# Optimization experiments

Measured on AMD Instinct MI355X. Metric: run time of the kernel, lower is better.

Reference implementation:

```python
import jax, jax.numpy as jnp
import numpy as np

NUM_PER_PATH = 16
MARGIN_INTRA = 0.1
MARGIN_INTER = 1.0


def setup_inputs() -> dict:
    key = jax.random.key(0)
    # [B, block_num, 1, 1, 2]; trailing dims must multiply to 2 (see _get_center view)
    path_fea = jax.random.normal(key, (131072, 64, 1, 1, 2), dtype=jnp.float32)
    return {"path_fea": path_fea}


def reference(path_fea):
    B, block = path_fea.shape[0], path_fea.shape[1]
    D = block * 2                     # flattened per-sample feature dim
    G = B // NUM_PER_PATH             # number of centers (groups)
    fea = path_fea.reshape(B, D)      # [B, D] (matches path_fea[j].view(-1))

    # center: mean over the NUM_PER_PATH samples of each group, per block
    # (identical math to the permute/view dance in _get_center)
    grouped = fea.reshape(G, NUM_PER_PATH, D)          # [G, P, D]
    center = jnp.mean(grouped, axis=1)                 # [G, D]

    # ---- inter loss: hinge on pairwise euclidean distances between centers ----
    sq = jnp.sum(center * center, axis=1)              # [G]
    gram = center @ center.T                           # [G, G]
    d2 = jnp.maximum(sq[:, None] + sq[None, :] - 2.0 * gram, 0.0)
    pair_mask = jnp.triu(jnp.ones((G, G), dtype=bool), k=1)  # i < j
    d = jnp.sqrt(jnp.where(pair_mask, d2, 1.0))        # safe sqrt off-mask
    hinge = jnp.maximum(MARGIN_INTER - d, 0.0) ** 2
    n_pairs = G * (G - 1) / 2.0
    inter_loss = jnp.sum(jnp.where(pair_mask, hinge, 0.0)) / n_pairs

    # ---- intra loss: hinge on distance of each sample to its group center ----
    diff = grouped - center[:, None, :]                # [G, P, D]
    di = jnp.sqrt(jnp.sum(diff * diff, axis=-1))       # [G, P]
    intra_loss = jnp.sum(jnp.maximum(di - MARGIN_INTRA, 0.0) ** 2) / (G * NUM_PER_PATH)

    return (inter_loss, intra_loss)
```

## Files before the change

kernel.cpp:

```cpp
#include <hip/hip_runtime.h>
#include <hip/hip_bf16.h>
#include <math.h>

#define B_ROWS   131072
#define D_DIM    128
#define P_SAMP   16
#define G_GROUPS 8192
#define T128     64
#define NTRI2    2080
#define K1_BLOCKS (G_GROUPS / 4)

typedef __bf16 bf16x8  __attribute__((ext_vector_type(8)));
typedef float  floatx4 __attribute__((ext_vector_type(4)));
typedef unsigned short u16x8 __attribute__((ext_vector_type(8)));


__device__ __forceinline__ float wave_red64(float v) {
    #pragma unroll
    for (int off = 32; off > 0; off >>= 1) v += __shfl_xor(v, off, 64);
    return v;
}

template <int CTRL>
__device__ __forceinline__ float dpp_ror_add(float v) {
    int r = __builtin_amdgcn_update_dpp(0, __builtin_bit_cast(int, v),
                                        CTRL, 0xf, 0xf, false);
    return v + __builtin_bit_cast(float, r);
}
__device__ __forceinline__ float row16_sum(float v) {
    v = dpp_ror_add<0x121>(v);
    v = dpp_ror_add<0x122>(v);
    v = dpp_ror_add<0x124>(v);
    v = dpp_ror_add<0x128>(v);
    return v;
}

__global__ __launch_bounds__(256) void k_center_intra(
    const float* __restrict__ x,
    uint2* __restrict__ cfrag,
    float* __restrict__ sq,
    float* __restrict__ partial,
    float* __restrict__ acc)
{
    const int wave = threadIdx.x >> 6;
    const int lane = threadIdx.x & 63;
    const int half = lane >> 5;
    const int c    = lane & 31;
    const int g    = blockIdx.x * 4 + wave;

    if (blockIdx.x == 0 && threadIdx.x == 0) acc[0] = 0.f;

    const float* base = x + (size_t)g * (P_SAMP * D_DIM) + half * D_DIM + c * 4;

    floatx4 v[8];
    #pragma unroll
    for (int l = 0; l < 8; ++l)
        v[l] = *(const floatx4*)(base + l * (2 * D_DIM));

    floatx4 cs = v[0];
    #pragma unroll
    for (int l = 1; l < 8; ++l) cs += v[l];
    #pragma unroll
    for (int k = 0; k < 4; ++k) cs[k] += __shfl_xor(cs[k], 32, 64);
    floatx4 ctr = cs * (1.0f / P_SAMP);

    float p[9];
    #pragma unroll
    for (int l = 0; l < 8; ++l) {
        floatx4 d = v[l] - ctr;
        p[l] = d[0]*d[0] + d[1]*d[1] + d[2]*d[2] + d[3]*d[3];
    }
    p[8] = ctr[0]*ctr[0] + ctr[1]*ctr[1] + ctr[2]*ctr[2] + ctr[3]*ctr[3];

    #pragma unroll
    for (int s = 0; s < 9; ++s) {
        p[s] = row16_sum(p[s]);
        p[s] += __shfl_xor(p[s], 16, 64);
    }

    if (half == 0) {
        unsigned int b0 = __builtin_bit_cast(unsigned short, (__bf16)ctr[0]);
        unsigned int b1 = __builtin_bit_cast(unsigned short, (__bf16)ctr[1]);
        unsigned int b2 = __builtin_bit_cast(unsigned short, (__bf16)ctr[2]);
        unsigned int b3 = __builtin_bit_cast(unsigned short, (__bf16)ctr[3]);
        uint2 pk;
        pk.x = (b1 << 16) | b0;
        pk.y = (b3 << 16) | b2;
        const int gran = (g >> 4) * 256 + (c >> 1) * 16 + (g & 15);
        cfrag[gran * 2 + (c & 1)] = pk;
    }
    if (lane == 0) sq[g] = p[8];

    float isum = 0.f;
    #pragma unroll
    for (int l = 0; l < 8; ++l) {
        float d = sqrtf(p[l]);
        float t = fmaxf(d - 0.1f, 0.f);
        isum += t * t;
    }
    isum += __shfl_xor(isum, 32, 64);

    __shared__ float sh[4];
    if (lane == 0) sh[wave] = isum;
    __syncthreads();
    if (threadIdx.x == 0)
        partial[blockIdx.x] = sh[0] + sh[1] + sh[2] + sh[3];
}

__global__ __launch_bounds__(256, 3) void k_inter(
    const u16x8* __restrict__ cfrag,
    const float* __restrict__ sq,
    float* __restrict__ acc)
{
    __shared__ u16x8 smemA[2048];

    const int bid = blockIdx.x;
    float sf = sqrtf(64.5f * 64.5f - 2.0f * (float)bid);
    int ti = (int)(64.5f - sf);
    if (ti < 0) ti = 0;
    if (ti > T128 - 1) ti = T128 - 1;
    #define TRI_OFF(i) ((i) * T128 - (((i) * ((i) - 1)) >> 1))
    while (ti > 0 && TRI_OFF(ti) > bid) --ti;
    while (ti < T128 - 1 && TRI_OFF(ti + 1) <= bid) ++ti;
    const int tj = ti + (bid - TRI_OFF(ti));
    #undef TRI_OFF

    const int t    = threadIdx.x;
    const int wave = t >> 6;
    const int lane = t & 63;
    const int wr   = wave >> 1;
    const int wc   = wave & 1;
    const int lrow = lane & 15;
    const int quad = lane >> 4;

    const int i0 = ti * 128 + wr * 64;
    const int j0 = tj * 128 + wc * 64;

    #define BIDX(nt, ks) (((size_t)tj * 8 + wc * 4 + (nt)) * 256 + ((ks) * 4 + quad) * 16 + lrow)
    bf16x8 bb[4][4];
    #pragma unroll
    for (int ks = 0; ks < 4; ++ks)
        #pragma unroll
        for (int nt = 0; nt < 4; ++nt)
            bb[ks][nt] = __builtin_bit_cast(bf16x8, cfrag[BIDX(nt, ks)]);
    #undef BIDX

    floatx4 sqi[4];
    float   sqj[4];
    #pragma unroll
    for (int mt = 0; mt < 4; ++mt)
        sqi[mt] = *(const floatx4*)(sq + i0 + mt * 16 + quad * 4);
    #pragma unroll
    for (int nt = 0; nt < 4; ++nt)
        sqj[nt] = sq[j0 + nt * 16 + lrow];

    const size_t abase = (size_t)ti * 2048;
    #pragma unroll
    for (int it = 0; it < 8; ++it)
        smemA[t + it * 256] = cfrag[abase + t + it * 256];
    __syncthreads();

    const bool bdiag = (ti == tj);
    if (bdiag && wr > wc) return;

    floatx4 c4[4][4] = {};

    #pragma unroll
    for (int ks = 0; ks < 4; ++ks) {
        bf16x8 a[4];
        const int go = (ks * 4 + quad) * 16 + lrow;
        #pragma unroll
        for (int mt = 0; mt < 4; ++mt)
            a[mt] = __builtin_bit_cast(bf16x8, smemA[(wr * 4 + mt) * 256 + go]);
        #pragma unroll
        for (int mt = 0; mt < 4; ++mt)
            #pragma unroll
            for (int nt = 0; nt < 4; ++nt)
                c4[mt][nt] = __builtin_amdgcn_mfma_f32_16x16x32_bf16(
                                a[mt], bb[ks][nt], c4[mt][nt], 0, 0, 0);
    }

    const bool qdiag = (bdiag && wr == wc);
    float hsum = 0.f;
    #pragma unroll
    for (int mt = 0; mt < 4; ++mt) {
        #pragma unroll
        for (int nt = 0; nt < 4; ++nt) {
            const int ib = i0 + mt * 16 + quad * 4;
            const int j  = j0 + nt * 16 + lrow;
            #pragma unroll
            for (int r = 0; r < 4; ++r) {
                if (qdiag && j <= ib + r) continue;
                float d2 = sqi[mt][r] + sqj[nt] - 2.0f * c4[mt][nt][r];
                if (d2 < 1.0f) {
                    float d = sqrtf(fmaxf(d2, 0.f));
                    float tt = 1.0f - d;
                    hsum += tt * tt;
                }
            }
        }
    }
    if (__ballot(hsum != 0.f)) {
        hsum = wave_red64(hsum);
        if (lane == 0) atomicAdd(acc, hsum);
    }
}

__global__ __launch_bounds__(256) void k_final(
    const float* __restrict__ acc,
    const float* __restrict__ partial,
    float* __restrict__ out)
{
    __shared__ float sh[4];
    float s = 0.f;
    for (int i = threadIdx.x; i < K1_BLOCKS; i += 256) s += partial[i];
    s = wave_red64(s);
    const int wave = threadIdx.x >> 6;
    const int lane = threadIdx.x & 63;
    if (lane == 0) sh[wave] = s;
    __syncthreads();
    if (threadIdx.x == 0) {
        const float n_pairs = (float)G_GROUPS * (float)(G_GROUPS - 1) * 0.5f;
        out[0] = acc[0] / n_pairs;
        out[1] = (sh[0] + sh[1] + sh[2] + sh[3]) / (float)B_ROWS;
    }
}

extern "C" void kernel_launch(void* const* d_in, const int* in_sizes, int n_in,
                              void* d_out, int out_size, void* d_ws, size_t ws_size,
                              hipStream_t stream) {
    const float* x = (const float*)d_in[0];
    float* out = (float*)d_out;

    float* acc     = (float*)d_ws;
    float* partial = (float*)((char*)d_ws + 256);
    float* sq      = (float*)((char*)d_ws + 16384);
    uint2* cfrag   = (uint2*)((char*)d_ws + 65536);

    k_center_intra<<<K1_BLOCKS, 256, 0, stream>>>(x, cfrag, sq, partial, acc);

    k_inter<<<NTRI2, 256, 0, stream>>>((const u16x8*)cfrag, sq, acc);

    k_final<<<1, 256, 0, stream>>>(acc, partial, out);
}
```

Measured before the change: 111.9 us.

## Make inter-center GEMM persistent per-wave with 64x64 tiles and register prefetch

Replaces the one-block-per-128x128-triangle-tile launch with 2048 persistent waves, each walking 64x64 upper-triangular tiles in a grid-stride loop. Operand fragments are loaded straight from global memory into registers and split into two K halves, so the next tile's loads overlap the current tile's MFMAs. This drops the shared-memory staging and the wasted lower-diagonal waves, and lowers launch bounds to 2 blocks per CU to fit the larger register set. The cost is more global/L2 traffic, because there is no reuse of A across waves, plus lower occupancy.

Result: slower. 118.3 us (+5.7%).

```diff
diff --git a/kernel.cpp b/kernel.cpp
--- a/kernel.cpp
+++ b/kernel.cpp
@@ -6,8 +6,9 @@
 #define D_DIM    128
 #define P_SAMP   16
 #define G_GROUPS 8192
-#define T128     64
-#define NTRI2    2080
+#define T64      128
+#define NTRI     8256
+#define NWAVES   2048
 #define K1_BLOCKS (G_GROUPS / 4)
 
 typedef __bf16 bf16x8  __attribute__((ext_vector_type(8)));
@@ -33,6 +34,19 @@
     v = dpp_ror_add<0x124>(v);
     v = dpp_ror_add<0x128>(v);
     return v;
+}
+
+__device__ __forceinline__ void decode_tri(int tid, int& ti, int& tj) {
+    float sf = sqrtf(128.5f * 128.5f - 2.0f * (float)tid);
+    int i = (int)(128.5f - sf);
+    if (i < 0) i = 0;
+    if (i > T64 - 1) i = T64 - 1;
+    #define TOFF(x) ((x) * T64 - (((x) * ((x) - 1)) >> 1))
+    while (i > 0 && TOFF(i) > tid) --i;
+    while (i < T64 - 1 && TOFF(i + 1) <= tid) ++i;
+    tj = i + (tid - TOFF(i));
+    #undef TOFF
+    ti = i;
 }
 
 __global__ __launch_bounds__(256) void k_center_intra(
@@ -107,99 +121,127 @@
         partial[blockIdx.x] = sh[0] + sh[1] + sh[2] + sh[3];
 }
 
-__global__ __launch_bounds__(256, 3) void k_inter(
+__global__ __launch_bounds__(256, 2) void k_inter(
     const u16x8* __restrict__ cfrag,
     const float* __restrict__ sq,
     float* __restrict__ acc)
 {
-    __shared__ u16x8 smemA[2048];
-
-    const int bid = blockIdx.x;
-    float sf = sqrtf(64.5f * 64.5f - 2.0f * (float)bid);
-    int ti = (int)(64.5f - sf);
-    if (ti < 0) ti = 0;
-    if (ti > T128 - 1) ti = T128 - 1;
-    #define TRI_OFF(i) ((i) * T128 - (((i) * ((i) - 1)) >> 1))
-    while (ti > 0 && TRI_OFF(ti) > bid) --ti;
-    while (ti < T128 - 1 && TRI_OFF(ti + 1) <= bid) ++ti;
-    const int tj = ti + (bid - TRI_OFF(ti));
-    #undef TRI_OFF
-
-    const int t    = threadIdx.x;
-    const int wave = t >> 6;
-    const int lane = t & 63;
-    const int wr   = wave >> 1;
-    const int wc   = wave & 1;
+    const int wid  = blockIdx.x * 4 + (threadIdx.x >> 6);
+    const int lane = threadIdx.x & 63;
     const int lrow = lane & 15;
     const int quad = lane >> 4;
 
-    const int i0 = ti * 128 + wr * 64;
-    const int j0 = tj * 128 + wc * 64;
-
-    #define BIDX(nt, ks) (((size_t)tj * 8 + wc * 4 + (nt)) * 256 + ((ks) * 4 + quad) * 16 + lrow)
-    bf16x8 bb[4][4];
-    #pragma unroll
-    for (int ks = 0; ks < 4; ++ks)
+    int tile = wid;
+    int ti, tj;
+    decode_tri(tile, ti, tj);
+
+    #define AIDX(TI, mt, ks) (((size_t)(TI) * 4 + (mt)) * 256 + ((ks) * 4 + quad) * 16 + lrow)
+    #define BIDX(TJ, nt, ks) (((size_t)(TJ) * 4 + (nt)) * 256 + ((ks) * 4 + quad) * 16 + lrow)
+
+    bf16x8 PA[2][4], PB[2][4], QA[2][4], QB[2][4];
+    #pragma unroll
+    for (int b = 0; b < 2; ++b) {
+        #pragma unroll
+        for (int mt = 0; mt < 4; ++mt) {
+            PA[b][mt] = __builtin_bit_cast(bf16x8, cfrag[AIDX(ti, mt, b)]);
+            QA[b][mt] = __builtin_bit_cast(bf16x8, cfrag[AIDX(ti, mt, b + 2)]);
+        }
+        #pragma unroll
+        for (int nt = 0; nt < 4; ++nt) {
+            PB[b][nt] = __builtin_bit_cast(bf16x8, cfrag[BIDX(tj, nt, b)]);
+            QB[b][nt] = __builtin_bit_cast(bf16x8, cfrag[BIDX(tj, nt, b + 2)]);
+        }
+    }
+
+    floatx4 c4[4][4] = {};
+    float hsum = 0.f;
+
+    for (;;) {
+        const int  ntile = tile + NWAVES;
+        const bool more  = (ntile < NTRI);
+        int nti = ti, ntj = tj;
+        if (more) decode_tri(ntile, nti, ntj);
+
+        #pragma unroll
+        for (int b = 0; b < 2; ++b)
+            #pragma unroll
+            for (int mt = 0; mt < 4; ++mt)
+                #pragma unroll
+                for (int nt = 0; nt < 4; ++nt)
+                    c4[mt][nt] = __builtin_amdgcn_mfma_f32_16x16x32_bf16(
+                                    PA[b][mt], PB[b][nt], c4[mt][nt], 0, 0, 0);
+
+        #pragma unroll
+        for (int b = 0; b < 2; ++b) {
+            #pragma unroll
+            for (int mt = 0; mt < 4; ++mt)
+                PA[b][mt] = __builtin_bit_cast(bf16x8, cfrag[AIDX(nti, mt, b)]);
+            #pragma unroll
+            for (int nt = 0; nt < 4; ++nt)
+                PB[b][nt] = __builtin_bit_cast(bf16x8, cfrag[BIDX(ntj, nt, b)]);
+        }
+
+        floatx4 sqi[4];
+        float   sqj[4];
+        #pragma unroll
+        for (int mt = 0; mt < 4; ++mt)
+            sqi[mt] = *(const floatx4*)(sq + ti * 64 + mt * 16 + quad * 4);
         #pragma unroll
         for (int nt = 0; nt < 4; ++nt)
-            bb[ks][nt] = __builtin_bit_cast(bf16x8, cfrag[BIDX(nt, ks)]);
-    #undef BIDX
-
-    floatx4 sqi[4];
-    float   sqj[4];
-    #pragma unroll
-    for (int mt = 0; mt < 4; ++mt)
-        sqi[mt] = *(const floatx4*)(sq + i0 + mt * 16 + quad * 4);
-    #pragma unroll
-    for (int nt = 0; nt < 4; ++nt)
-        sqj[nt] = sq[j0 + nt * 16 + lrow];
-
-    const size_t abase = (size_t)ti * 2048;
-    #pragma unroll
-    for (int it = 0; it < 8; ++it)
-        smemA[t + it * 256] = cfrag[abase + t + it * 256];
-    __syncthreads();
-
-    const bool bdiag = (ti == tj);
-    if (bdiag && wr > wc) return;
-
-    floatx4 c4[4][4] = {};
-
-    #pragma unroll
-    for (int ks = 0; ks < 4; ++ks) {
-        bf16x8 a[4];
-        const int go = (ks * 4 + quad) * 16 + lrow;
-        #pragma unroll
-        for (int mt = 0; mt < 4; ++mt)
-            a[mt] = __builtin_bit_cast(bf16x8, smemA[(wr * 4 + mt) * 256 + go]);
-        #pragma unroll
-        for (int mt = 0; mt < 4; ++mt)
+            sqj[nt] = sq[tj * 64 + nt * 16 + lrow];
+
+        #pragma unroll
+        for (int b = 0; b < 2; ++b)
+            #pragma unroll
+            for (int mt = 0; mt < 4; ++mt)
+                #pragma unroll
+                for (int nt = 0; nt < 4; ++nt)
+                    c4[mt][nt] = __builtin_amdgcn_mfma_f32_16x16x32_bf16(
+                                    QA[b][mt], QB[b][nt], c4[mt][nt], 0, 0, 0);
+
+        #pragma unroll
+        for (int b = 0; b < 2; ++b) {
+            #pragma unroll
+            for (int mt = 0; mt < 4; ++mt)
+                QA[b][mt] = __builtin_bit_cast(bf16x8, cfrag[AIDX(nti, mt, b + 2)]);
             #pragma unroll
             for (int nt = 0; nt < 4; ++nt)
-                c4[mt][nt] = __builtin_amdgcn_mfma_f32_16x16x32_bf16(
-                                a[mt], bb[ks][nt], c4[mt][nt], 0, 0, 0);
-    }
-
-    const bool qdiag = (bdiag && wr == wc);
-    float hsum = 0.f;
-    #pragma unroll
-    for (int mt = 0; mt < 4; ++mt) {
-        #pragma unroll
-        for (int nt = 0; nt < 4; ++nt) {
-            const int ib = i0 + mt * 16 + quad * 4;
-            const int j  = j0 + nt * 16 + lrow;
-            #pragma unroll
-            for (int r = 0; r < 4; ++r) {
-                if (qdiag && j <= ib + r) continue;
-                float d2 = sqi[mt][r] + sqj[nt] - 2.0f * c4[mt][nt][r];
-                if (d2 < 1.0f) {
-                    float d = sqrtf(fmaxf(d2, 0.f));
-                    float tt = 1.0f - d;
-                    hsum += tt * tt;
+                QB[b][nt] = __builtin_bit_cast(bf16x8, cfrag[BIDX(ntj, nt, b + 2)]);
+        }
+
+        const bool diag = (ti == tj);
+        const int  i0   = ti * 64;
+        const int  j0   = tj * 64;
+        #pragma unroll
+        for (int mt = 0; mt < 4; ++mt) {
+            #pragma unroll
+            for (int nt = 0; nt < 4; ++nt) {
+                const int ib = i0 + mt * 16 + quad * 4;
+                const int j  = j0 + nt * 16 + lrow;
+                #pragma unroll
+                for (int r = 0; r < 4; ++r) {
+                    if (diag && j <= ib + r) continue;
+                    float d2 = sqi[mt][r] + sqj[nt] - 2.0f * c4[mt][nt][r];
+                    if (d2 < 1.0f) {
+                        float d = sqrtf(fmaxf(d2, 0.f));
+                        float tt = 1.0f - d;
+                        hsum += tt * tt;
+                    }
                 }
             }
         }
-    }
+        #pragma unroll
+        for (int mt = 0; mt < 4; ++mt)
+            #pragma unroll
+            for (int nt = 0; nt < 4; ++nt)
+                c4[mt][nt] = (floatx4)(0.0f);
+
+        if (!more) break;
+        tile = ntile; ti = nti; tj = ntj;
+    }
+    #undef AIDX
+    #undef BIDX
+
     if (__ballot(hsum != 0.f)) {
         hsum = wave_red64(hsum);
         if (lane == 0) atomicAdd(acc, hsum);
@@ -239,7 +281,7 @@
 
     k_center_intra<<<K1_BLOCKS, 256, 0, stream>>>(x, cfrag, sq, partial, acc);
 
-    k_inter<<<NTRI2, 256, 0, stream>>>((const u16x8*)cfrag, sq, acc);
+    k_inter<<<NWAVES / 4, 256, 0, stream>>>((const u16x8*)cfrag, sq, acc);
 
     k_final<<<1, 256, 0, stream>>>(acc, partial, out);
 }
```
